# Kernel tuning notes

Measured on AMD Instinct MI355X. Metric: run time of the kernel, lower is better.

Reference implementation:

```python
import jax, jax.numpy as jnp
import numpy as np

ROWS, COLS = 10, 4
B, N = 65536, 16


def setup_inputs() -> dict:
    key = jax.random.key(0)
    kx, kc = jax.random.split(key)
    # 0.5 scale keeps trace(x^(rows+1))^cols finite in float32 (spectral radius ~2)
    x = jax.random.normal(kx, (B, N, N), dtype=jnp.float32) * 0.5
    # kaiming_normal_ on a 2D (rows, cols) tensor: std = sqrt(2 / fan_in), fan_in = cols
    coef = jax.random.normal(kc, (ROWS, COLS), dtype=jnp.float32) * np.float32(np.sqrt(2.0 / COLS))
    return {"x": x, "coef": coef}


def reference(x, coef):
    # x: [B, N, N]; coef: [rows, cols]
    rows, cols = coef.shape
    n = x.shape[-1] * x.shape[-2]  # numel per sample

    A0 = jnp.matmul(x, x)  # x^2, the first a_series entry

    def step(A, _):
        # original records trace(a_series[i]) = trace(x^(i+2)), then advances the power
        tr = jnp.trace(A, axis1=-2, axis2=-1)  # [B]
        return jnp.matmul(x, A), tr

    _, traces = jax.lax.scan(step, A0, None, length=rows)  # traces: [rows, B]
    t = traces.T  # [B, rows]

    jexp = jnp.arange(1, cols + 1, dtype=jnp.float32)  # j+1 exponents
    iexp = jnp.arange(rows, dtype=jnp.float32)
    # feature[b, i, j] = trace(x^(i+2))^(j+1) / n^(i+j+1)
    denom = jnp.float32(n) ** (iexp[:, None] + jexp[None, :])  # [rows, cols]
    feats = (t[:, :, None] ** jexp[None, None, :]) / denom  # [B, rows, cols]

    # terms = coef * feats, summed over (rows, cols) per sample -> [B]
    return jnp.einsum('rc,brc->b', coef, feats)
```

## Files before the change

kernel.cpp:

```cpp
#include <hip/hip_runtime.h>

typedef __fp16 f16x4 __attribute__((ext_vector_type(4)));
typedef __fp16 f16x2 __attribute__((ext_vector_type(2)));
typedef float f32x4 __attribute__((ext_vector_type(4)));

template <int CTRL>
__device__ __forceinline__ float dpp_add(float v) {
    int s = __builtin_amdgcn_update_dpp(0, __float_as_int(v), CTRL, 0xf, 0xf, true);
    return v + __int_as_float(s);
}

__device__ __forceinline__ float wave_sum_uniform(float v) {
    v = dpp_add<0x111>(v);
    v = dpp_add<0x112>(v);
    v = dpp_add<0x114>(v);
    v = dpp_add<0x118>(v);
    v = dpp_add<0x142>(v);
    v = dpp_add<0x143>(v);
    return __int_as_float(__builtin_amdgcn_readlane(__float_as_int(v), 63));
}

__global__ __launch_bounds__(256) void acoef_kernel(
    const float* __restrict__ x,
    const float* __restrict__ coef,
    float* __restrict__ out)
{
    const int lane = threadIdx.x & 63;
    const int wave = threadIdx.x >> 6;
    const int b = blockIdx.x * 4 + wave;
    const float* __restrict__ xb = x + (size_t)b * 256;

    const int n = lane & 15;
    const int q = lane >> 4;

    const float4 a = *(const float4*)(xb + n * 16 + 4 * q);
    f16x2 alo = __builtin_amdgcn_cvt_pkrtz(a.x, a.y);
    f16x2 ahi = __builtin_amdgcn_cvt_pkrtz(a.z, a.w);
    f16x4 xA = __builtin_shufflevector(alo, ahi, 0, 1, 2, 3);

    float b0 = xb[(4 * q + 0) * 16 + n];
    float b1 = xb[(4 * q + 1) * 16 + n];
    float b2 = xb[(4 * q + 2) * 16 + n];
    float b3 = xb[(4 * q + 3) * 16 + n];
    f16x2 blo = __builtin_amdgcn_cvt_pkrtz(b0, b1);
    f16x2 bhi = __builtin_amdgcn_cvt_pkrtz(b2, b3);
    f16x4 xB = __builtin_shufflevector(blo, bhi, 0, 1, 2, 3);

    const f32x4 zero = {0.f, 0.f, 0.f, 0.f};
    f32x4 acc = __builtin_amdgcn_mfma_f32_16x16x16f16(xA, xB, zero, 0, 0, 0);

    const bool diagsel = ((n >> 2) == q);
    float tr[10];

    #pragma unroll
    for (int s = 0; s < 10; ++s) {
        float selA = (n & 1) ? acc[1] : acc[0];
        float selB = (n & 1) ? acc[3] : acc[2];
        float dv   = (n & 2) ? selB : selA;
        tr[s] = diagsel ? dv : 0.0f;

        if (s < 9) {
            f16x2 lo = __builtin_amdgcn_cvt_pkrtz(acc[0], acc[1]);
            f16x2 hi = __builtin_amdgcn_cvt_pkrtz(acc[2], acc[3]);
            f16x4 bf = __builtin_shufflevector(lo, hi, 0, 1, 2, 3);
            acc = __builtin_amdgcn_mfma_f32_16x16x16f16(xA, bf, zero, 0, 0, 0);
        }
    }

    constexpr float SC[10] = {0x1p0f,  0x1p-8f,  0x1p-16f, 0x1p-24f, 0x1p-32f,
                              0x1p-40f, 0x1p-48f, 0x1p-56f, 0x1p-64f, 0x1p-72f};
    float result = 0.0f;
    #pragma unroll
    for (int s = 0; s < 10; ++s) {
        float t  = wave_sum_uniform(tr[s]);
        float sv = t * 0x1p-8f;
        float h = fmaf(sv, coef[s * 4 + 3], coef[s * 4 + 2]);
        h = fmaf(sv, h, coef[s * 4 + 1]);
        h = fmaf(sv, h, coef[s * 4 + 0]);
        result = fmaf(sv * h, SC[s], result);
    }
    if (lane == 0) out[b] = result;
}

extern "C" void kernel_launch(void* const* d_in, const int* in_sizes, int n_in,
                              void* d_out, int out_size, void* d_ws, size_t ws_size,
                              hipStream_t stream) {
    const float* x    = (const float*)d_in[0];
    const float* coef = (const float*)d_in[1];
    float* out        = (float*)d_out;
    const int B = in_sizes[0] / 256;
    acoef_kernel<<<dim3(B / 4), dim3(256), 0, stream>>>(x, coef, out);
}
```

Before: 103.8 us.

## Reduce trace sums via MFMA with ones/selector matrices instead of DPP reductions

Replaces the ten separate wave-wide DPP reductions of per-step trace contributions with packed fp16 values fed through MFMA instructions, using a selector matrix and a ones matrix to sum across lanes. Each of the three MFMA pairs produces four traces, which are spread across lanes; each lane evaluates one polynomial term and a final small DPP reduction combines them. This cuts the number of cross-lane reduction instructions. In exchange, the trace sums are now accumulated from fp16-rounded partial values (and the intermediate c1 is rounded again), which lowers precision and risks overflow for large traces.

After: 99.42 us. 1.04x faster.

```diff
diff --git a/kernel.cpp b/kernel.cpp
--- a/kernel.cpp
+++ b/kernel.cpp
@@ -4,20 +4,17 @@
 typedef __fp16 f16x2 __attribute__((ext_vector_type(2)));
 typedef float f32x4 __attribute__((ext_vector_type(4)));
 
+__device__ __forceinline__ f16x4 cat(f16x2 lo, f16x2 hi) {
+    return __builtin_shufflevector(lo, hi, 0, 1, 2, 3);
+}
+__device__ __forceinline__ f16x2 u2h(unsigned v) {
+    union { unsigned u; f16x2 h; } x; x.u = v; return x.h;
+}
+
 template <int CTRL>
 __device__ __forceinline__ float dpp_add(float v) {
     int s = __builtin_amdgcn_update_dpp(0, __float_as_int(v), CTRL, 0xf, 0xf, true);
     return v + __int_as_float(s);
-}
-
-__device__ __forceinline__ float wave_sum_uniform(float v) {
-    v = dpp_add<0x111>(v);
-    v = dpp_add<0x112>(v);
-    v = dpp_add<0x114>(v);
-    v = dpp_add<0x118>(v);
-    v = dpp_add<0x142>(v);
-    v = dpp_add<0x143>(v);
-    return __int_as_float(__builtin_amdgcn_readlane(__float_as_int(v), 63));
 }
 
 __global__ __launch_bounds__(256) void acoef_kernel(
@@ -34,51 +31,69 @@
     const int q = lane >> 4;
 
     const float4 a = *(const float4*)(xb + n * 16 + 4 * q);
-    f16x2 alo = __builtin_amdgcn_cvt_pkrtz(a.x, a.y);
-    f16x2 ahi = __builtin_amdgcn_cvt_pkrtz(a.z, a.w);
-    f16x4 xA = __builtin_shufflevector(alo, ahi, 0, 1, 2, 3);
+    f16x4 xA = cat(__builtin_amdgcn_cvt_pkrtz(a.x, a.y),
+                   __builtin_amdgcn_cvt_pkrtz(a.z, a.w));
 
     float b0 = xb[(4 * q + 0) * 16 + n];
     float b1 = xb[(4 * q + 1) * 16 + n];
     float b2 = xb[(4 * q + 2) * 16 + n];
     float b3 = xb[(4 * q + 3) * 16 + n];
-    f16x2 blo = __builtin_amdgcn_cvt_pkrtz(b0, b1);
-    f16x2 bhi = __builtin_amdgcn_cvt_pkrtz(b2, b3);
-    f16x4 xB = __builtin_shufflevector(blo, bhi, 0, 1, 2, 3);
+    f16x4 xB = cat(__builtin_amdgcn_cvt_pkrtz(b0, b1),
+                   __builtin_amdgcn_cvt_pkrtz(b2, b3));
 
     const f32x4 zero = {0.f, 0.f, 0.f, 0.f};
     f32x4 acc = __builtin_amdgcn_mfma_f32_16x16x16f16(xA, xB, zero, 0, 0, 0);
 
     const bool diagsel = ((n >> 2) == q);
-    float tr[10];
+
+    f16x2 prpk[6];
+    float trf = 0.0f;
 
     #pragma unroll
     for (int s = 0; s < 10; ++s) {
         float selA = (n & 1) ? acc[1] : acc[0];
         float selB = (n & 1) ? acc[3] : acc[2];
         float dv   = (n & 2) ? selB : selA;
-        tr[s] = diagsel ? dv : 0.0f;
+        float tr   = diagsel ? dv : 0.0f;
+        if (s & 1) prpk[s >> 1] = __builtin_amdgcn_cvt_pkrtz(trf, tr);
+        else       trf = tr;
 
         if (s < 9) {
-            f16x2 lo = __builtin_amdgcn_cvt_pkrtz(acc[0], acc[1]);
-            f16x2 hi = __builtin_amdgcn_cvt_pkrtz(acc[2], acc[3]);
-            f16x4 bf = __builtin_shufflevector(lo, hi, 0, 1, 2, 3);
+            f16x4 bf = cat(__builtin_amdgcn_cvt_pkrtz(acc[0], acc[1]),
+                           __builtin_amdgcn_cvt_pkrtz(acc[2], acc[3]));
             acc = __builtin_amdgcn_mfma_f32_16x16x16f16(xA, bf, zero, 0, 0, 0);
         }
     }
+    prpk[5] = u2h(0u);
 
-    constexpr float SC[10] = {0x1p0f,  0x1p-8f,  0x1p-16f, 0x1p-24f, 0x1p-32f,
-                              0x1p-40f, 0x1p-48f, 0x1p-56f, 0x1p-64f, 0x1p-72f};
+    unsigned slo = (n == 0 ? 0x3C00u : 0u) | (n == 1 ? 0x3C000000u : 0u);
+    unsigned shi = (n == 2 ? 0x3C00u : 0u) | (n == 3 ? 0x3C000000u : 0u);
+    f16x4 selB = cat(u2h(slo), u2h(shi));
+    f16x4 onesA = cat(u2h(0x3C003C00u), u2h(0x3C003C00u));
+
     float result = 0.0f;
     #pragma unroll
-    for (int s = 0; s < 10; ++s) {
-        float t  = wave_sum_uniform(tr[s]);
+    for (int p = 0; p < 3; ++p) {
+        f16x4 Ap = cat(prpk[2 * p], prpk[2 * p + 1]);
+        f32x4 c1 = __builtin_amdgcn_mfma_f32_16x16x16f16(Ap, selB, zero, 0, 0, 0);
+        f16x4 Bp = cat(__builtin_amdgcn_cvt_pkrtz(c1[0], c1[1]),
+                       __builtin_amdgcn_cvt_pkrtz(c1[2], c1[3]));
+        f32x4 c2 = __builtin_amdgcn_mfma_f32_16x16x16f16(onesA, Bp, zero, 0, 0, 0);
+        float t = c2[0];
+
+        int s = 4 * p + n;
+        int idx = s > 9 ? 9 : s;
+        const float4 c = *(const float4*)(coef + 4 * idx);
         float sv = t * 0x1p-8f;
-        float h = fmaf(sv, coef[s * 4 + 3], coef[s * 4 + 2]);
-        h = fmaf(sv, h, coef[s * 4 + 1]);
-        h = fmaf(sv, h, coef[s * 4 + 0]);
-        result = fmaf(sv * h, SC[s], result);
+        float h = fmaf(sv, c.w, c.z);
+        h = fmaf(sv, h, c.y);
+        h = fmaf(sv, h, c.x);
+        float scl = __int_as_float((127 - 8 * s) << 23);
+        result = fmaf(sv * h, scl, result);
     }
+
+    result = dpp_add<0xB1>(result);
+    result = dpp_add<0x4E>(result);
     if (lane == 0) out[b] = result;
 }
 
```
